# Performance work log

Hardware: AMD Instinct MI355X
Metric: run time of the kernel (lower is better)

## Reference

```python
import jax, jax.numpy as jnp
import numpy as np

B, N, DIM, H = 4, 128, 512, 8
EPS = 1e-5

def _lin(k, fan_in, fan_out):
    kw, kb = jax.random.split(k)
    w = jax.random.normal(kw, (fan_in, fan_out), jnp.float32) * 0.02
    b = jax.random.normal(kb, (fan_out,), jnp.float32) * 0.02
    return w, b

def setup_inputs() -> dict:
    key = jax.random.key(0)
    ks = jax.random.split(key, 12)
    node_features = jax.random.normal(ks[0], (B, N, DIM), jnp.float32)
    edge_features = jax.random.normal(ks[1], (B, N, N, DIM), jnp.float32)
    adjacency_weights = jax.random.uniform(ks[2], (B, N, N), jnp.float32)
    Wn_w, Wn_b = _lin(ks[3], DIM, DIM)
    We1_w, We1_b = _lin(ks[4], 3 * DIM, DIM)
    We2_w, We2_b = _lin(ks[5], DIM, H)
    Wm_w, Wm_b = _lin(ks[6], DIM, DIM)
    Wu1_w, Wu1_b = _lin(ks[7], 3 * DIM, DIM)
    Wu2_w, Wu2_b = _lin(ks[8], DIM, DIM)
    Wo_w, Wo_b = _lin(ks[9], DIM, DIM)
    ln_g = jnp.ones((DIM,), jnp.float32)
    ln_b = jnp.zeros((DIM,), jnp.float32)
    return dict(node_features=node_features, edge_features=edge_features,
                adjacency_weights=adjacency_weights,
                Wn_w=Wn_w, Wn_b=Wn_b, We1_w=We1_w, We1_b=We1_b,
                We2_w=We2_w, We2_b=We2_b, Wm_w=Wm_w, Wm_b=Wm_b,
                Wu1_w=Wu1_w, Wu1_b=Wu1_b, Wu2_w=Wu2_w, Wu2_b=Wu2_b,
                Wo_w=Wo_w, Wo_b=Wo_b, ln_g=ln_g, ln_b=ln_b)

def _layernorm(x, g, b):
    mu = jnp.mean(x, axis=-1, keepdims=True)
    var = jnp.var(x, axis=-1, keepdims=True)
    return (x - mu) * jax.lax.rsqrt(var + EPS) * g + b

def reference(node_features, edge_features, adjacency_weights,
              Wn_w, Wn_b, We1_w, We1_b, We2_w, We2_b, Wm_w, Wm_b,
              Wu1_w, Wu1_b, Wu2_w, Wu2_b, Wo_w, Wo_b, ln_g, ln_b):
    b, n, d = node_features.shape
    h = node_features @ Wn_w + Wn_b                       # (B,N,D)
    h_i = jnp.broadcast_to(h[:, :, None, :], (b, n, n, d))
    h_j = jnp.broadcast_to(h[:, None, :, :], (b, n, n, d))
    edge_input = jnp.concatenate([h_i, h_j, edge_features], axis=-1)  # (B,N,N,3D)
    # edge attention MLP
    e = jax.nn.leaky_relu(edge_input @ We1_w + We1_b, negative_slope=0.2)
    attn = e @ We2_w + We2_b                              # (B,N,N,H)
    attn = jax.nn.softmax(attn, axis=2)                   # softmax over j
    attn = attn * adjacency_weights[..., None]
    # messages: W_msg applied to h_j == W_msg(h) broadcast; aggregate with mean attn
    messages = h @ Wm_w + Wm_b                            # (B,N,D)
    attn_mean = jnp.mean(attn, axis=-1)                   # (B,N,N)
    aggregated = jnp.einsum('bij,bjd->bid', attn_mean, messages)
    updated_nodes = _layernorm(node_features + (aggregated @ Wo_w + Wo_b), ln_g, ln_b)
    # edge update MLP (exact GELU as in torch default)
    u = jax.nn.gelu(edge_input @ Wu1_w + Wu1_b, approximate=False)
    updated_edges = edge_features + (u @ Wu2_w + Wu2_b)
    return updated_nodes, updated_edges
```

## Files before the change

kernel.cpp:

```cpp
#include <hip/hip_runtime.h>
#include <hip/hip_bf16.h>


typedef __bf16  bf16x8 __attribute__((ext_vector_type(8)));
typedef float   f32x4  __attribute__((ext_vector_type(4)));
typedef __hip_bfloat16 bfloat;

#define AS1 __attribute__((address_space(1)))
#define AS3 __attribute__((address_space(3)))

__device__ __forceinline__ void g2l16(const void* g, void* l) {
  __builtin_amdgcn_global_load_lds((AS1 void*)g, (AS3 void*)l, 16, 0, 0);
}

__device__ __forceinline__ float ldf(const void* p, size_t i, int f) {
  return f ? ((const float*)p)[i] : __bfloat162float(((const bfloat*)p)[i]);
}
__device__ __forceinline__ void stf(void* p, size_t i, float v, int f) {
  if (f) ((float*)p)[i] = v;
  else   ((bfloat*)p)[i] = __float2bfloat16(v);
}

__device__ __forceinline__ float gelu_f(float x) {
  float y = 0.7978845608028654f * (x + 0.044715f * x * x * x);
  float e = __expf(2.0f * y);
  float t = 1.0f - 2.0f / (e + 1.0f);
  return 0.5f * x * (1.0f + t);
}

__global__ __launch_bounds__(256) void detect_dtype(const unsigned short* nu, int* flag) {
  __shared__ int bad;
  if (threadIdx.x == 0) bad = 0;
  __syncthreads();
  int local = 0;
  for (int i = threadIdx.x; i < 4096; i += 256) {
    int ex = (nu[i] >> 7) & 0xFF;
    if (ex >= 0xC0) local = 1;
  }
  if (local) atomicOr(&bad, 1);
  __syncthreads();
  if (threadIdx.x == 0) *flag = bad;
}

__global__ __launch_bounds__(256) void cvt_edge(const float* E, const int* flag, void* dout) {
  if (*flag == 0) return;
  const int e = blockIdx.x & 7;
  const int x = blockIdx.x >> 3;
  const int m = x >> 5;
  const int h = (x >> 4) & 1;
  const int s = x & 15;
  const int c = 2 * e + 16 * m + h;
  const int t = threadIdx.x;
  const int rloc = s * 4 + (t >> 6);
  const int c8 = t & 63;
  const float* src = E + ((size_t)c * 64 + rloc) * 512 + (size_t)c8 * 8;
  f32x4 lo = *(const f32x4*)src;
  f32x4 hi = *(const f32x4*)(src + 4);
  bf16x8 v;
  v[0] = (__bf16)lo[0]; v[1] = (__bf16)lo[1]; v[2] = (__bf16)lo[2]; v[3] = (__bf16)lo[3];
  v[4] = (__bf16)hi[0]; v[5] = (__bf16)hi[1]; v[6] = (__bf16)hi[2]; v[7] = (__bf16)hi[3];
  char* eb = (char*)dout + 1048576;
  *(bf16x8*)(eb + (size_t)c * 131072 + (size_t)rloc * 1024 + (size_t)c8 * 16) = v;
}

__global__ __launch_bounds__(256) void transpose3(const void* We1, const void* Wu1,
                                                  const void* Wu2, const void* Wm,
                                                  const int* flag,
                                                  bfloat* WtA, bfloat* WtB, bfloat* WtC,
                                                  bfloat* WtD, bfloat* WtE, bfloat* WtF,
                                                  bfloat* WtG, bfloat* WtH) {
  const int f = *flag;
  int idx = blockIdx.x * 256 + threadIdx.x;
  int m = idx >> 18;
  int r = idx & 262143;
  int n = r >> 9, k = r & 511;
  size_t si = (size_t)k * 512 + n;
  float v;
  bfloat* dst;
  switch (m) {
    case 0:  v = ldf(We1, 524288 + si, f); dst = WtA; break;
    case 1:  v = ldf(Wu1, 524288 + si, f); dst = WtB; break;
    case 2:  v = ldf(Wu2, si, f);          dst = WtC; break;
    case 3:  v = ldf(We1, si, f);          dst = WtD; break;
    case 4:  v = ldf(We1, 262144 + si, f); dst = WtE; break;
    case 5:  v = ldf(Wu1, si, f);          dst = WtF; break;
    case 6:  v = ldf(Wu1, 262144 + si, f); dst = WtG; break;
    default: v = ldf(Wm, si, f);           dst = WtH; break;
  }
  dst[(size_t)n * 512 + k] = __float2bfloat16(v);
}

__global__ __launch_bounds__(256) void small_gemm(const void* A, int amode, const void* W,
                                                  size_t woff, const void* bias,
                                                  const int* flag, float* out, bfloat* outb) {
  const int f = *flag;
  const int af = amode ? 1 : f;
  __shared__ float sA[4][512];
  const int t = threadIdx.x;
  const int r0 = blockIdx.x * 4;
  for (int idx = t; idx < 2048; idx += 256)
    sA[idx >> 9][idx & 511] = ldf(A, (size_t)(r0 + (idx >> 9)) * 512 + (idx & 511), af);
  __syncthreads();
  float acc0[4] = {0.f, 0.f, 0.f, 0.f}, acc1[4] = {0.f, 0.f, 0.f, 0.f};
#pragma unroll 4
  for (int k = 0; k < 512; ++k) {
    float w0 = ldf(W, woff + (size_t)k * 512 + t, f);
    float w1 = ldf(W, woff + (size_t)k * 512 + t + 256, f);
#pragma unroll
    for (int r = 0; r < 4; ++r) {
      acc0[r] += sA[r][k] * w0;
      acc1[r] += sA[r][k] * w1;
    }
  }
  float b0 = bias ? ldf(bias, t, f) : 0.f;
  float b1 = bias ? ldf(bias, t + 256, f) : 0.f;
#pragma unroll
  for (int r = 0; r < 4; ++r) {
    float o0 = acc0[r] + b0, o1 = acc1[r] + b1;
    out[(size_t)(r0 + r) * 512 + t] = o0;
    out[(size_t)(r0 + r) * 512 + t + 256] = o1;
    if (outb) {
      outb[(size_t)(r0 + r) * 512 + t] = __float2bfloat16(o0);
      outb[(size_t)(r0 + r) * 512 + t + 256] = __float2bfloat16(o1);
    }
  }
}

__global__ __launch_bounds__(256) void fused5_mfma(const bfloat* hb, const bfloat* WtD,
                                                   const bfloat* WtE, const bfloat* WtF,
                                                   const bfloat* WtG, const bfloat* WtH,
                                                   const void* We1b, const void* Wu1b,
                                                   const void* Wmb, const int* flag,
                                                   float* P1, float* Q1, float* P2, float* Q2,
                                                   float* msgv) {
  const int fl = *flag;
  __shared__ __align__(16) char smem[49152];
  f32x4 acc[4][4];
#pragma unroll
  for (int mi = 0; mi < 4; ++mi)
#pragma unroll
    for (int ni = 0; ni < 4; ++ni) acc[mi][ni] = (f32x4){0.f, 0.f, 0.f, 0.f};

  const int bid = blockIdx.x;
  const int g = bid >> 4, rb = (bid >> 2) & 3, cbv = bid & 3;
  const bfloat* Wt;
  const void* bias = nullptr;
  float* out;
  switch (g) {
    case 0:  Wt = WtD; bias = We1b; out = P1; break;
    case 1:  Wt = WtE; out = Q1; break;
    case 2:  Wt = WtF; bias = Wu1b; out = P2; break;
    case 3:  Wt = WtG; out = Q2; break;
    default: Wt = WtH; bias = Wmb; out = msgv; break;
  }
  const bfloat* Ag = hb + (size_t)rb * 65536;
  const bfloat* Bg = Wt + (size_t)cbv * 65536;

  const int t = threadIdx.x, lane = t & 63, wave = t >> 6;
  const int wrow = wave >> 1, wcol = wave & 1;
  const int l15 = lane & 15, q = lane >> 4;

  const int row0 = t >> 2, p0 = t & 3, g0 = p0 ^ ((row0 >> 1) & 3);
  const int row1 = 64 + row0, g1 = p0 ^ ((row1 >> 1) & 3);
  const char* srcA0 = (const char*)(Ag + (size_t)row0 * 512 + g0 * 8);
  const char* srcA1 = (const char*)(Ag + (size_t)row1 * 512 + g1 * 8);
  const char* srcB0 = (const char*)(Bg + (size_t)row0 * 512 + g0 * 8);
  const char* srcB1 = (const char*)(Bg + (size_t)row1 * 512 + g1 * 8);
  const int dst0 = wave * 1024, dst1 = 4096 + wave * 1024;

  auto stage = [&](int kt2, int sel2) {
    const int koff = kt2 * 64;
    char* dA = smem + sel2 * 8192;
    char* dB = smem + 24576 + sel2 * 8192;
    g2l16(srcA0 + koff, dA + dst0);
    g2l16(srcA1 + koff, dA + dst1);
    g2l16(srcB0 + koff, dB + dst0);
    g2l16(srcB1 + koff, dB + dst1);
  };
  stage(0, 0);
  stage(1, 1);

  const int swz = (q ^ ((l15 >> 1) & 3)) * 16;
  const int fA = (wrow * 64 + l15) * 64 + swz;
  const int fB = (wcol * 64 + l15) * 64 + swz;

#pragma unroll
  for (int kt = 0; kt < 16; ++kt) {
    if (kt < 15) asm volatile("s_waitcnt vmcnt(4)" ::: "memory");
    else         asm volatile("s_waitcnt vmcnt(0)" ::: "memory");
    __builtin_amdgcn_s_barrier();
    if (kt < 14) stage(kt + 2, (kt + 2) % 3);
    const char* A = smem + (kt % 3) * 8192;
    const char* B = smem + 24576 + (kt % 3) * 8192;
    bf16x8 afr[4], bfr[4];
#pragma unroll
    for (int mi = 0; mi < 4; ++mi) afr[mi] = *(const bf16x8*)(A + fA + mi * 1024);
#pragma unroll
    for (int ni = 0; ni < 4; ++ni) bfr[ni] = *(const bf16x8*)(B + fB + ni * 1024);
#pragma unroll
    for (int mi = 0; mi < 4; ++mi)
#pragma unroll
      for (int ni = 0; ni < 4; ++ni)
        acc[mi][ni] =
            __builtin_amdgcn_mfma_f32_16x16x32_bf16(afr[mi], bfr[ni], acc[mi][ni], 0, 0, 0);
  }

  float bv[4];
#pragma unroll
  for (int ni = 0; ni < 4; ++ni)
    bv[ni] = bias ? ldf(bias, (size_t)cbv * 128 + wcol * 64 + ni * 16 + l15, fl) : 0.f;
#pragma unroll
  for (int mi = 0; mi < 4; ++mi)
#pragma unroll
    for (int rr = 0; rr < 4; ++rr) {
      const int j = wrow * 64 + mi * 16 + q * 4 + rr;
#pragma unroll
      for (int ni = 0; ni < 4; ++ni) {
        const int cc = wcol * 64 + ni * 16 + l15;
        out[(size_t)(rb * 128 + j) * 512 + cbv * 128 + cc] = acc[mi][ni][rr] + bv[ni];
      }
    }
}

__global__ __launch_bounds__(256) void k3_edge_mlp(const void* E, const bfloat* WtA,
                                                   const bfloat* WtB, const float* P1,
                                                   const float* Q1, const float* P2,
                                                   const float* Q2, const void* We2,
                                                   const int* flag, float* logits4, void* dout) {
  const int f = *flag;
  __shared__ __align__(16) char smem[77824];
  f32x4 accA[4][4], accU[4][4];
#pragma unroll
  for (int mi = 0; mi < 4; ++mi)
#pragma unroll
    for (int ni = 0; ni < 4; ++ni) {
      accA[mi][ni] = (f32x4){0.f, 0.f, 0.f, 0.f};
      accU[mi][ni] = (f32x4){0.f, 0.f, 0.f, 0.f};
    }

  const int idx0 = blockIdx.x;
  const int bm = (idx0 >> 5) * 8 + (idx0 & 7);
  const int cb = (idx0 >> 3) & 3;
  const int blockcol = cb * 128;
  const bfloat* BgA = WtA + (size_t)cb * 65536;
  const bfloat* BgU = WtB + (size_t)cb * 65536;
  const bfloat* Eb = (const bfloat*)E;
  const char* eb = (const char*)dout + 1048576;

  const int t = threadIdx.x, lane = t & 63, wave = t >> 6;
  const int wrow = wave >> 1, wcol = wave & 1;
  const int l15 = lane & 15, q = lane >> 4;

  for (int idx = t; idx < 2048; idx += 256) {
    const int n = idx >> 7, k = idx & 127;
    float v = (n < 8) ? ldf(We2, (size_t)(blockcol + k) * 8 + n, f) : 0.f;
    *(bfloat*)(smem + 73728 + (size_t)n * 256 + (((k >> 3) ^ n) * 16) + (k & 7) * 2) =
        __float2bfloat16(v);
  }

  const int row0 = t >> 2, p0 = t & 3, g0 = p0 ^ ((row0 >> 1) & 3);
  const int row1 = 64 + row0, g1 = p0 ^ ((row1 >> 1) & 3);
  const char* srcA0;
  const char* srcA1;
  const int gr0 = bm * 128 + row0, gr1 = gr0 + 64;
  if (f) {
    srcA0 = eb + (size_t)(gr0 >> 6) * 131072 + (size_t)(gr0 & 63) * 1024 + (size_t)g0 * 16;
    srcA1 = eb + (size_t)(gr1 >> 6) * 131072 + (size_t)(gr1 & 63) * 1024 + (size_t)g1 * 16;
  } else {
    srcA0 = (const char*)Eb + ((size_t)gr0 * 512 + g0 * 8) * 2;
    srcA1 = (const char*)Eb + ((size_t)gr1 * 512 + g1 * 8) * 2;
  }
  const int dstA0 = wave * 1024, dstA1 = 4096 + wave * 1024;

  const char* srcB[4];
  int dstB[4];
#pragma unroll
  for (int c = 0; c < 4; ++c) {
    const int idx = c * 256 + t;
    const int row = idx >> 2, p = idx & 3, gg = p ^ ((row >> 1) & 3);
    const bfloat* base =
        (row < 128) ? (BgA + (size_t)row * 512) : (BgU + (size_t)(row - 128) * 512);
    srcB[c] = (const char*)base + gg * 16;
    dstB[c] = (c * 256 + wave * 64) * 16;
  }

  auto stage = [&](int kt2, int sel2) {
    const int koff = kt2 * 64;
    char* dA = smem + sel2 * 8192;
    char* dB = smem + 24576 + sel2 * 16384;
    g2l16(srcA0 + koff, dA + dstA0);
    g2l16(srcA1 + koff, dA + dstA1);
#pragma unroll
    for (int c = 0; c < 4; ++c) g2l16(srcB[c] + koff, dB + dstB[c]);
  };
  stage(0, 0);
  stage(1, 1);

  const int swz = (q ^ ((l15 >> 1) & 3)) * 16;
  const int fA = (wrow * 64 + l15) * 64 + swz;
  const int fB = (wcol * 64 + l15) * 64 + swz;

#pragma unroll
  for (int kt = 0; kt < 16; ++kt) {
    if (kt < 15) asm volatile("s_waitcnt vmcnt(6)" ::: "memory");
    else         asm volatile("s_waitcnt vmcnt(0)" ::: "memory");
    __builtin_amdgcn_s_barrier();
    if (kt < 14) stage(kt + 2, (kt + 2) % 3);
    const char* A = smem + (kt % 3) * 8192;
    const char* B = smem + 24576 + (kt % 3) * 16384;
    bf16x8 afr[4], bfrA[4], bfrU[4];
#pragma unroll
    for (int mi = 0; mi < 4; ++mi) afr[mi] = *(const bf16x8*)(A + fA + mi * 1024);
#pragma unroll
    for (int ni = 0; ni < 4; ++ni) bfrA[ni] = *(const bf16x8*)(B + fB + ni * 1024);
#pragma unroll
    for (int mi = 0; mi < 4; ++mi)
#pragma unroll
      for (int ni = 0; ni < 4; ++ni)
        accA[mi][ni] =
            __builtin_amdgcn_mfma_f32_16x16x32_bf16(afr[mi], bfrA[ni], accA[mi][ni], 0, 0, 0);
#pragma unroll
    for (int ni = 0; ni < 4; ++ni) bfrU[ni] = *(const bf16x8*)(B + 8192 + fB + ni * 1024);
#pragma unroll
    for (int mi = 0; mi < 4; ++mi)
#pragma unroll
      for (int ni = 0; ni < 4; ++ni)
        accU[mi][ni] =
            __builtin_amdgcn_mfma_f32_16x16x32_bf16(afr[mi], bfrU[ni], accU[mi][ni], 0, 0, 0);
  }

  const int b = bm >> 7;
  float pv1[4], pv2[4];
#pragma unroll
  for (int ni = 0; ni < 4; ++ni) {
    const size_t o = (size_t)bm * 512 + blockcol + wcol * 64 + ni * 16 + l15;
    pv1[ni] = P1[o];
    pv2[ni] = P2[o];
  }
  __syncthreads();

#pragma unroll
  for (int mi = 0; mi < 4; ++mi)
#pragma unroll
    for (int rr = 0; rr < 4; ++rr) {
      const int j = wrow * 64 + mi * 16 + q * 4 + rr;
#pragma unroll
      for (int ni = 0; ni < 4; ++ni) {
        const int cc = wcol * 64 + ni * 16 + l15;
        const int c = blockcol + cc;
        float x = accU[mi][ni][rr] + pv2[ni] + Q2[((size_t)b * 128 + j) * 512 + c];
        *(bfloat*)(smem + (size_t)j * 256 + (((cc >> 3) ^ (j & 15)) * 16) + (cc & 7) * 2) =
            __float2bfloat16(gelu_f(x));
      }
    }
  __syncthreads();
  {
    char* ubase = (char*)dout + (f ? (1048576 + 65536) : 524288);
    const size_t blkstride = f ? 131072 : 65536;
#pragma unroll
    for (int rd = 0; rd < 8; ++rd) {
      const int j = rd * 16 + (t >> 4);
      const int ch = t & 15;
      f32x4 v = *(const f32x4*)(smem + (size_t)j * 256 + ((ch ^ (j & 15)) * 16));
      const size_t m = (size_t)bm * 128 + j;
      *(f32x4*)(ubase + (m >> 6) * blkstride + (m & 63) * 1024 + (size_t)blockcol * 2 +
                (size_t)ch * 16) = v;
    }
  }
  __syncthreads();

#pragma unroll
  for (int mi = 0; mi < 4; ++mi)
#pragma unroll
    for (int rr = 0; rr < 4; ++rr) {
      const int j = wrow * 64 + mi * 16 + q * 4 + rr;
#pragma unroll
      for (int ni = 0; ni < 4; ++ni) {
        const int cc = wcol * 64 + ni * 16 + l15;
        const int c = blockcol + cc;
        float x = accA[mi][ni][rr] + pv1[ni] + Q1[((size_t)b * 128 + j) * 512 + c];
        float e4 = (x >= 0.f) ? x : 0.2f * x;
        *(bfloat*)(smem + (size_t)j * 256 + (((cc >> 3) ^ (j & 15)) * 16) + (cc & 7) * 2) =
            __float2bfloat16(e4);
      }
    }
  __syncthreads();
  {
    f32x4 acc2[2];
    acc2[0] = (f32x4){0.f, 0.f, 0.f, 0.f};
    acc2[1] = (f32x4){0.f, 0.f, 0.f, 0.f};
    const int jb = wave * 32;
#pragma unroll
    for (int ks = 0; ks < 4; ++ks) {
      const int gA = ((ks * 4 + q) ^ l15) * 16;
      bf16x8 a0 = *(const bf16x8*)(smem + (size_t)(jb + l15) * 256 + gA);
      bf16x8 a1 = *(const bf16x8*)(smem + (size_t)(jb + 16 + l15) * 256 + gA);
      bf16x8 bb = *(const bf16x8*)(smem + 73728 + (size_t)l15 * 256 + gA);
      acc2[0] = __builtin_amdgcn_mfma_f32_16x16x32_bf16(a0, bb, acc2[0], 0, 0, 0);
      acc2[1] = __builtin_amdgcn_mfma_f32_16x16x32_bf16(a1, bb, acc2[1], 0, 0, 0);
    }
#pragma unroll
    for (int mi2 = 0; mi2 < 2; ++mi2)
#pragma unroll
      for (int rr = 0; rr < 4; ++rr) {
        if (l15 < 8) {
          const int j = jb + mi2 * 16 + q * 4 + rr;
          logits4[(((size_t)cb * 512 + bm) * 128 + j) * 8 + l15] = acc2[mi2][rr];
        }
      }
  }
}

__global__ __launch_bounds__(512) void k6_edge_out(const bfloat* WtC, const void* Wu2b,
                                                   const void* E, const int* flag, void* dout) {
  const int f = *flag;
  __shared__ __align__(16) char smem[110592];
  f32x4 acc[2][8];
#pragma unroll
  for (int mi = 0; mi < 2; ++mi)
#pragma unroll
    for (int ni = 0; ni < 8; ++ni) acc[mi][ni] = (f32x4){0.f, 0.f, 0.f, 0.f};

  const int e = blockIdx.x & 7;
  const int x = blockIdx.x >> 3;
  const int bm = 2 * e + 16 * (x >> 1) + (x & 1);
  const int t = threadIdx.x;
  const int lane = t & 63;
  const int wave = t >> 6;
  const int wm = wave >> 2, wn = wave & 3;
  const int l15 = lane & 15;
  const int q = lane >> 4;
  const size_t r0 = (size_t)bm * 64;
  const char* ua = (const char*)dout +
                   (f ? (1048576 + (size_t)bm * 131072 + 65536) : (524288 + (size_t)bm * 65536));

  const int iA = t & 255;
  const int rowA = iA >> 2, pA = iA & 3, gA = pA ^ ((rowA >> 1) & 3);
  const char* srcA = ua + (size_t)rowA * 1024 + (size_t)gA * 16;
  const int dstA = (wave & 3) * 1024;
  const char* srcB[4];
  int dstB[4];
#pragma unroll
  for (int c = 0; c < 4; ++c) {
    const int idx = c * 512 + t;
    const int row = idx >> 2, p = idx & 3, g = p ^ ((row >> 1) & 3);
    srcB[c] = (const char*)WtC + ((size_t)row * 512 + g * 8) * 2;
    dstB[c] = (c * 512 + wave * 64) * 16;
  }

  auto stage = [&](int kt2, int sel2) {
    const int koff = kt2 * 64;
    char* dA = smem + sel2 * 4096;
    char* dB = smem + 12288 + sel2 * 32768;
    g2l16(srcA + koff, dA + dstA);
#pragma unroll
    for (int c = 0; c < 4; ++c) g2l16(srcB[c] + koff, dB + dstB[c]);
  };

  stage(0, 0);
  stage(1, 1);

  const int swz = (q ^ ((l15 >> 1) & 3)) * 16;
  const int fAo = (wm * 32 + l15) * 64 + swz;
  const int fBo = (wn * 128 + l15) * 64 + swz;

#pragma unroll
  for (int kt = 0; kt < 16; ++kt) {
    if (kt < 15) asm volatile("s_waitcnt vmcnt(5)" ::: "memory");
    else         asm volatile("s_waitcnt vmcnt(0)" ::: "memory");
    __builtin_amdgcn_s_barrier();
    if (kt < 14) stage(kt + 2, (kt + 2) % 3);
    const char* sA = smem + (kt % 3) * 4096;
    const char* sB = smem + 12288 + (kt % 3) * 32768;
    bf16x8 afr[2], bfr[8];
#pragma unroll
    for (int mi = 0; mi < 2; ++mi) afr[mi] = *(const bf16x8*)(sA + fAo + mi * 1024);
#pragma unroll
    for (int ni = 0; ni < 8; ++ni) bfr[ni] = *(const bf16x8*)(sB + fBo + ni * 1024);
#pragma unroll
    for (int mi = 0; mi < 2; ++mi)
#pragma unroll
      for (int ni = 0; ni < 8; ++ni)
        acc[mi][ni] = __builtin_amdgcn_mfma_f32_16x16x32_bf16(afr[mi], bfr[ni], acc[mi][ni], 0, 0, 0);
  }
  float wb[8];
#pragma unroll
  for (int ni = 0; ni < 8; ++ni) wb[ni] = ldf(Wu2b, wn * 128 + ni * 16 + l15, f);
  const bfloat* eres = (const bfloat*)((const char*)dout + 1048576 + (size_t)bm * 131072);
#pragma unroll
  for (int mi = 0; mi < 2; ++mi)
#pragma unroll
    for (int rr = 0; rr < 4; ++rr) {
      const int j = wm * 32 + mi * 16 + q * 4 + rr;
#pragma unroll
      for (int ni = 0; ni < 8; ++ni) {
        const int c = wn * 128 + ni * 16 + l15;
        float r = f ? __bfloat162float(eres[(size_t)j * 512 + c])
                    : __bfloat162float(((const bfloat*)E)[(r0 + j) * 512 + c]);
        acc[mi][ni][rr] += wb[ni] + r;
      }
    }
  __syncthreads();
#pragma unroll
  for (int mi = 0; mi < 2; ++mi)
#pragma unroll
    for (int rr = 0; rr < 4; ++rr) {
      const int j = wm * 32 + mi * 16 + q * 4 + rr;
      const size_t row = r0 + j;
#pragma unroll
      for (int ni = 0; ni < 8; ++ni) {
        const int c = wn * 128 + ni * 16 + l15;
        stf(dout, 262144 + row * 512 + c, acc[mi][ni][rr], f);
      }
    }
}

__global__ __launch_bounds__(128) void softmax_mean(const float* logits4, const void* adj,
                                                    const int* flag, float* amean) {
  const int f = *flag;
  const int bi = blockIdx.x;
  const int j = threadIdx.x;
  const int wv = j >> 6;
  __shared__ float sred[2][8];
  f32x4 v0 = (f32x4){0.f, 0.f, 0.f, 0.f}, v1 = (f32x4){0.f, 0.f, 0.f, 0.f};
#pragma unroll
  for (int s = 0; s < 4; ++s) {
    const float* p = logits4 + (((size_t)s * 512 + bi) * 128 + j) * 8;
    v0 += *(const f32x4*)p;
    v1 += *(const f32x4*)(p + 4);
  }
  float xv[8], m[8];
#pragma unroll
  for (int k = 0; k < 4; ++k) { xv[k] = v0[k]; xv[4 + k] = v1[k]; }
#pragma unroll
  for (int h = 0; h < 8; ++h) m[h] = xv[h];
#pragma unroll
  for (int o = 1; o < 64; o <<= 1)
#pragma unroll
    for (int h = 0; h < 8; ++h) m[h] = fmaxf(m[h], __shfl_xor(m[h], o));
  if ((j & 63) == 0) {
#pragma unroll
    for (int h = 0; h < 8; ++h) sred[wv][h] = m[h];
  }
  __syncthreads();
  float ex[8], s8[8];
#pragma unroll
  for (int h = 0; h < 8; ++h) {
    float mx = fmaxf(sred[0][h], sred[1][h]);
    ex[h] = __expf(xv[h] - mx);
    s8[h] = ex[h];
  }
#pragma unroll
  for (int o = 1; o < 64; o <<= 1)
#pragma unroll
    for (int h = 0; h < 8; ++h) s8[h] += __shfl_xor(s8[h], o);
  __syncthreads();
  if ((j & 63) == 0) {
#pragma unroll
    for (int h = 0; h < 8; ++h) sred[wv][h] = s8[h];
  }
  __syncthreads();
  float macc = 0.f;
#pragma unroll
  for (int h = 0; h < 8; ++h) macc += ex[h] / (sred[0][h] + sred[1][h]);
  amean[(size_t)bi * 128 + j] = macc * 0.125f * ldf(adj, (size_t)bi * 128 + j, f);
}

__global__ __launch_bounds__(256) void node_fused(const float* amean, const float* msg,
                                                  const void* Wo, const void* Wob,
                                                  const void* node, const void* lng,
                                                  const void* lnb, const int* flag, void* dout) {
  const int f = *flag;
  const int r0 = blockIdx.x * 4;
  const int b = r0 >> 7;
  const int t = threadIdx.x;
  const int lane = t & 63, wave = t >> 6;
  __shared__ float am[512];
  __shared__ float sAgg[4][512];
  __shared__ float sw[4][4];
  __shared__ float sw2[4][4];
  am[t] = amean[(size_t)r0 * 128 + t];
  am[t + 256] = amean[(size_t)r0 * 128 + t + 256];
  __syncthreads();
  float a0[4] = {0.f, 0.f, 0.f, 0.f}, a1[4] = {0.f, 0.f, 0.f, 0.f};
#pragma unroll 2
  for (int jj = 0; jj < 128; ++jj) {
    const float* mr = msg + ((size_t)b * 128 + jj) * 512;
    float m0 = mr[t], m1 = mr[t + 256];
#pragma unroll
    for (int r = 0; r < 4; ++r) {
      a0[r] += am[r * 128 + jj] * m0;
      a1[r] += am[r * 128 + jj] * m1;
    }
  }
#pragma unroll
  for (int r = 0; r < 4; ++r) { sAgg[r][t] = a0[r]; sAgg[r][t + 256] = a1[r]; }
  __syncthreads();
  float v0[4] = {0.f, 0.f, 0.f, 0.f}, v1[4] = {0.f, 0.f, 0.f, 0.f};
  if (f) {
    const float* W = (const float*)Wo;
#pragma unroll 2
    for (int k = 0; k < 512; ++k) {
      float w0 = W[(size_t)k * 512 + t], w1 = W[(size_t)k * 512 + t + 256];
#pragma unroll
      for (int r = 0; r < 4; ++r) { v0[r] += sAgg[r][k] * w0; v1[r] += sAgg[r][k] * w1; }
    }
  } else {
    const bfloat* W = (const bfloat*)Wo;
#pragma unroll 2
    for (int k = 0; k < 512; ++k) {
      float w0 = __bfloat162float(W[(size_t)k * 512 + t]);
      float w1 = __bfloat162float(W[(size_t)k * 512 + t + 256]);
#pragma unroll
      for (int r = 0; r < 4; ++r) { v0[r] += sAgg[r][k] * w0; v1[r] += sAgg[r][k] * w1; }
    }
  }
  float wob0 = ldf(Wob, t, f), wob1 = ldf(Wob, t + 256, f);
#pragma unroll
  for (int r = 0; r < 4; ++r) {
    v0[r] += wob0 + ldf(node, (size_t)(r0 + r) * 512 + t, f);
    v1[r] += wob1 + ldf(node, (size_t)(r0 + r) * 512 + t + 256, f);
  }
  float s[4];
#pragma unroll
  for (int r = 0; r < 4; ++r) s[r] = v0[r] + v1[r];
#pragma unroll
  for (int o = 1; o < 64; o <<= 1)
#pragma unroll
    for (int r = 0; r < 4; ++r) s[r] += __shfl_xor(s[r], o);
  if (lane == 0) {
#pragma unroll
    for (int r = 0; r < 4; ++r) sw[wave][r] = s[r];
  }
  __syncthreads();
  float mean[4];
#pragma unroll
  for (int r = 0; r < 4; ++r)
    mean[r] = (sw[0][r] + sw[1][r] + sw[2][r] + sw[3][r]) * (1.f / 512.f);
#pragma unroll
  for (int r = 0; r < 4; ++r) {
    float d0 = v0[r] - mean[r], d1 = v1[r] - mean[r];
    s[r] = d0 * d0 + d1 * d1;
  }
#pragma unroll
  for (int o = 1; o < 64; o <<= 1)
#pragma unroll
    for (int r = 0; r < 4; ++r) s[r] += __shfl_xor(s[r], o);
  if (lane == 0) {
#pragma unroll
    for (int r = 0; r < 4; ++r) sw2[wave][r] = s[r];
  }
  __syncthreads();
  float g0v = ldf(lng, t, f), g1v = ldf(lng, t + 256, f);
  float b0v = ldf(lnb, t, f), b1v = ldf(lnb, t + 256, f);
#pragma unroll
  for (int r = 0; r < 4; ++r) {
    float var = (sw2[0][r] + sw2[1][r] + sw2[2][r] + sw2[3][r]) * (1.f / 512.f);
    float inv = rsqrtf(var + 1e-5f);
    stf(dout, (size_t)(r0 + r) * 512 + t, (v0[r] - mean[r]) * inv * g0v + b0v, f);
    stf(dout, (size_t)(r0 + r) * 512 + t + 256, (v1[r] - mean[r]) * inv * g1v + b1v, f);
  }
}

extern "C" void kernel_launch(void* const* d_in, const int* in_sizes, int n_in, void* d_out,
                              int out_size, void* d_ws, size_t ws_size, hipStream_t stream) {
  (void)in_sizes; (void)n_in; (void)out_size; (void)ws_size;
  const void* node = d_in[0];
  const void* edge = d_in[1];
  const void* adj = d_in[2];
  const void* Wn_w = d_in[3];
  const void* Wn_b = d_in[4];
  const void* We1_w = d_in[5];
  const void* We1_b = d_in[6];
  const void* We2_w = d_in[7];
  const void* Wm_w = d_in[9];
  const void* Wm_b = d_in[10];
  const void* Wu1_w = d_in[11];
  const void* Wu1_b = d_in[12];
  const void* Wu2_w = d_in[13];
  const void* Wu2_b = d_in[14];
  const void* Wo_w = d_in[15];
  const void* Wo_b = d_in[16];
  const void* ln_g = d_in[17];
  const void* ln_b = d_in[18];

  char* w = (char*)d_ws;
  int* flag = (int*)w;        w += 256;
  float* h = (float*)w;       w += 262144 * 4;
  float* P1 = (float*)w;      w += 262144 * 4;
  float* Q1 = (float*)w;      w += 262144 * 4;
  float* P2 = (float*)w;      w += 262144 * 4;
  float* Q2 = (float*)w;      w += 262144 * 4;
  float* msg = (float*)w;     w += 262144 * 4;
  float* logits4 = (float*)w; w += (size_t)4 * 524288 * 4;
  float* amean = (float*)w;   w += 65536 * 4;
  bfloat* WtA = (bfloat*)w;   w += 262144 * 2;
  bfloat* WtB = (bfloat*)w;   w += 262144 * 2;
  bfloat* WtC = (bfloat*)w;   w += 262144 * 2;
  bfloat* WtD = (bfloat*)w;   w += 262144 * 2;
  bfloat* WtE = (bfloat*)w;   w += 262144 * 2;
  bfloat* WtF = (bfloat*)w;   w += 262144 * 2;
  bfloat* WtG = (bfloat*)w;   w += 262144 * 2;
  bfloat* WtH = (bfloat*)w;   w += 262144 * 2;
  bfloat* hb = (bfloat*)w;    w += 262144 * 2;

  detect_dtype<<<1, 256, 0, stream>>>((const unsigned short*)node, flag);
  cvt_edge<<<16384, 256, 0, stream>>>((const float*)edge, flag, d_out);
  transpose3<<<8192, 256, 0, stream>>>(We1_w, Wu1_w, Wu2_w, Wm_w, flag, WtA, WtB, WtC,
                                       WtD, WtE, WtF, WtG, WtH);
  small_gemm<<<128, 256, 0, stream>>>(node, 0, Wn_w, 0, Wn_b, flag, h, hb);
  fused5_mfma<<<80, 256, 0, stream>>>(hb, WtD, WtE, WtF, WtG, WtH, We1_b, Wu1_b, Wm_b, flag,
                                      P1, Q1, P2, Q2, msg);
  k3_edge_mlp<<<2048, 256, 0, stream>>>(edge, WtA, WtB, P1, Q1, P2, Q2, We2_w, flag,
                                        logits4, d_out);
  softmax_mean<<<512, 128, 0, stream>>>(logits4, adj, flag, amean);
  node_fused<<<128, 256, 0, stream>>>(amean, msg, Wo_w, Wo_b, node, ln_g, ln_b, flag, d_out);
  k6_edge_out<<<1024, 512, 0, stream>>>(WtC, Wu2_b, edge, flag, d_out);
}
```

Before: 823.6 us.

## Split edge MLP blocks by branch, stage GELU output in workspace, tile weight transpose

```diff
diff --git a/kernel.cpp b/kernel.cpp
--- a/kernel.cpp
+++ b/kernel.cpp
@@ -63,31 +63,49 @@
   *(bf16x8*)(eb + (size_t)c * 131072 + (size_t)rloc * 1024 + (size_t)c8 * 16) = v;
 }
 
-__global__ __launch_bounds__(256) void transpose3(const void* We1, const void* Wu1,
+__global__ __launch_bounds__(256) void transpose8(const void* We1, const void* Wu1,
                                                   const void* Wu2, const void* Wm,
                                                   const int* flag,
                                                   bfloat* WtA, bfloat* WtB, bfloat* WtC,
                                                   bfloat* WtD, bfloat* WtE, bfloat* WtF,
                                                   bfloat* WtG, bfloat* WtH) {
   const int f = *flag;
-  int idx = blockIdx.x * 256 + threadIdx.x;
-  int m = idx >> 18;
-  int r = idx & 262143;
-  int n = r >> 9, k = r & 511;
-  size_t si = (size_t)k * 512 + n;
-  float v;
+  __shared__ float sT[64][65];
+  const int m = blockIdx.x >> 6;
+  const int tile = blockIdx.x & 63;
+  const int k0 = (tile >> 3) * 64, n0 = (tile & 7) * 64;
+  const void* src;
+  size_t woff = 0;
   bfloat* dst;
   switch (m) {
-    case 0:  v = ldf(We1, 524288 + si, f); dst = WtA; break;
-    case 1:  v = ldf(Wu1, 524288 + si, f); dst = WtB; break;
-    case 2:  v = ldf(Wu2, si, f);          dst = WtC; break;
-    case 3:  v = ldf(We1, si, f);          dst = WtD; break;
-    case 4:  v = ldf(We1, 262144 + si, f); dst = WtE; break;
-    case 5:  v = ldf(Wu1, si, f);          dst = WtF; break;
-    case 6:  v = ldf(Wu1, 262144 + si, f); dst = WtG; break;
-    default: v = ldf(Wm, si, f);           dst = WtH; break;
-  }
-  dst[(size_t)n * 512 + k] = __float2bfloat16(v);
+    case 0:  src = We1; woff = 524288; dst = WtA; break;
+    case 1:  src = Wu1; woff = 524288; dst = WtB; break;
+    case 2:  src = Wu2; dst = WtC; break;
+    case 3:  src = We1; dst = WtD; break;
+    case 4:  src = We1; woff = 262144; dst = WtE; break;
+    case 5:  src = Wu1; dst = WtF; break;
+    case 6:  src = Wu1; woff = 262144; dst = WtG; break;
+    default: src = Wm; dst = WtH; break;
+  }
+  const int t = threadIdx.x;
+#pragma unroll
+  for (int p = 0; p < 4; ++p) {
+    const int r = p * 16 + (t >> 4);
+    const int cs = (t & 15) * 4;
+    const size_t base = woff + (size_t)(k0 + r) * 512 + n0 + cs;
+#pragma unroll
+    for (int i = 0; i < 4; ++i) sT[r][cs + i] = ldf(src, base + i, f);
+  }
+  __syncthreads();
+#pragma unroll
+  for (int p = 0; p < 2; ++p) {
+    const int n = p * 32 + (t >> 3);
+    const int ks = (t & 7) * 8;
+    bf16x8 v;
+#pragma unroll
+    for (int i = 0; i < 8; ++i) v[i] = (__bf16)sT[ks + i][n];
+    *(bf16x8*)(dst + (size_t)(n0 + n) * 512 + k0 + ks) = v;
+  }
 }
 
 __global__ __launch_bounds__(256) void small_gemm(const void* A, int amode, const void* W,
@@ -226,40 +244,36 @@
                                                    const bfloat* WtB, const float* P1,
                                                    const float* Q1, const float* P2,
                                                    const float* Q2, const void* We2,
-                                                   const int* flag, float* logits4, void* dout) {
+                                                   const int* flag, float* logits4,
+                                                   bfloat* uws, void* dout) {
   const int f = *flag;
-  __shared__ __align__(16) char smem[77824];
-  f32x4 accA[4][4], accU[4][4];
+  __shared__ __align__(16) char smem[53248];
+  f32x4 acc[4][4];
 #pragma unroll
   for (int mi = 0; mi < 4; ++mi)
 #pragma unroll
-    for (int ni = 0; ni < 4; ++ni) {
-      accA[mi][ni] = (f32x4){0.f, 0.f, 0.f, 0.f};
-      accU[mi][ni] = (f32x4){0.f, 0.f, 0.f, 0.f};
-    }
+    for (int ni = 0; ni < 4; ++ni) acc[mi][ni] = (f32x4){0.f, 0.f, 0.f, 0.f};
 
   const int idx0 = blockIdx.x;
-  const int bm = (idx0 >> 5) * 8 + (idx0 & 7);
-  const int cb = (idx0 >> 3) & 3;
-  const int blockcol = cb * 128;
-  const bfloat* BgA = WtA + (size_t)cb * 65536;
-  const bfloat* BgU = WtB + (size_t)cb * 65536;
+  const int bm = (idx0 >> 6) * 8 + (idx0 & 7);
+  const int bn = (idx0 >> 3) & 7;
+  const bool attn = bn < 4;
+  const bfloat* Bg = attn ? WtA + (size_t)bn * 65536 : WtB + (size_t)(bn - 4) * 65536;
   const bfloat* Eb = (const bfloat*)E;
   const char* eb = (const char*)dout + 1048576;
 
-  const int t = threadIdx.x, lane = t & 63, wave = t >> 6;
+  const int t = threadIdx.x;
+  const int lane = t & 63;
+  const int wave = t >> 6;
   const int wrow = wave >> 1, wcol = wave & 1;
-  const int l15 = lane & 15, q = lane >> 4;
-
-  for (int idx = t; idx < 2048; idx += 256) {
-    const int n = idx >> 7, k = idx & 127;
-    float v = (n < 8) ? ldf(We2, (size_t)(blockcol + k) * 8 + n, f) : 0.f;
-    *(bfloat*)(smem + 73728 + (size_t)n * 256 + (((k >> 3) ^ n) * 16) + (k & 7) * 2) =
-        __float2bfloat16(v);
-  }
+  const int l15 = lane & 15;
+  const int q = lane >> 4;
+  const int blockcol = (attn ? bn : (bn - 4)) * 128;
 
   const int row0 = t >> 2, p0 = t & 3, g0 = p0 ^ ((row0 >> 1) & 3);
   const int row1 = 64 + row0, g1 = p0 ^ ((row1 >> 1) & 3);
+  const char* srcB0 = (const char*)Bg + ((size_t)row0 * 512 + g0 * 8) * 2;
+  const char* srcB1 = (const char*)Bg + ((size_t)row1 * 512 + g1 * 8) * 2;
   const char* srcA0;
   const char* srcA1;
   const int gr0 = bm * 128 + row0, gr1 = gr0 + 64;
@@ -270,93 +284,87 @@
     srcA0 = (const char*)Eb + ((size_t)gr0 * 512 + g0 * 8) * 2;
     srcA1 = (const char*)Eb + ((size_t)gr1 * 512 + g1 * 8) * 2;
   }
-  const int dstA0 = wave * 1024, dstA1 = 4096 + wave * 1024;
-
-  const char* srcB[4];
-  int dstB[4];
-#pragma unroll
-  for (int c = 0; c < 4; ++c) {
-    const int idx = c * 256 + t;
-    const int row = idx >> 2, p = idx & 3, gg = p ^ ((row >> 1) & 3);
-    const bfloat* base =
-        (row < 128) ? (BgA + (size_t)row * 512) : (BgU + (size_t)(row - 128) * 512);
-    srcB[c] = (const char*)base + gg * 16;
-    dstB[c] = (c * 256 + wave * 64) * 16;
-  }
+  const int dst0 = wave * 1024;
+  const int dst1 = 4096 + wave * 1024;
 
   auto stage = [&](int kt2, int sel2) {
+    char* dA = smem + sel2 * 8192;
+    char* dB = smem + 24576 + sel2 * 8192;
     const int koff = kt2 * 64;
-    char* dA = smem + sel2 * 8192;
-    char* dB = smem + 24576 + sel2 * 16384;
-    g2l16(srcA0 + koff, dA + dstA0);
-    g2l16(srcA1 + koff, dA + dstA1);
-#pragma unroll
-    for (int c = 0; c < 4; ++c) g2l16(srcB[c] + koff, dB + dstB[c]);
+    g2l16(srcA0 + koff, dA + dst0);
+    g2l16(srcA1 + koff, dA + dst1);
+    g2l16(srcB0 + koff, dB + dst0);
+    g2l16(srcB1 + koff, dB + dst1);
   };
+
   stage(0, 0);
   stage(1, 1);
 
-  const int swz = (q ^ ((l15 >> 1) & 3)) * 16;
-  const int fA = (wrow * 64 + l15) * 64 + swz;
-  const int fB = (wcol * 64 + l15) * 64 + swz;
+  if (attn) {
+    for (int idx = t; idx < 2048; idx += 256) {
+      const int n = idx >> 7, k = idx & 127;
+      float v = (n < 8) ? ldf(We2, (size_t)(blockcol + k) * 8 + n, f) : 0.f;
+      *(bfloat*)(smem + 49152 + (size_t)n * 256 + (((k >> 3) ^ n) * 16) + (k & 7) * 2) =
+          __float2bfloat16(v);
+    }
+  }
+
+  const int swzf = (q ^ ((l15 >> 1) & 3)) * 16;
+  const int fA = (wrow * 64 + l15) * 64 + swzf;
+  const int fB = (wcol * 64 + l15) * 64 + swzf;
 
 #pragma unroll
   for (int kt = 0; kt < 16; ++kt) {
-    if (kt < 15) asm volatile("s_waitcnt vmcnt(6)" ::: "memory");
+    if (kt < 15) asm volatile("s_waitcnt vmcnt(4)" ::: "memory");
     else         asm volatile("s_waitcnt vmcnt(0)" ::: "memory");
     __builtin_amdgcn_s_barrier();
     if (kt < 14) stage(kt + 2, (kt + 2) % 3);
     const char* A = smem + (kt % 3) * 8192;
-    const char* B = smem + 24576 + (kt % 3) * 16384;
-    bf16x8 afr[4], bfrA[4], bfrU[4];
+    const char* B = smem + 24576 + (kt % 3) * 8192;
+    bf16x8 afr[4], bfr[4];
 #pragma unroll
     for (int mi = 0; mi < 4; ++mi) afr[mi] = *(const bf16x8*)(A + fA + mi * 1024);
 #pragma unroll
-    for (int ni = 0; ni < 4; ++ni) bfrA[ni] = *(const bf16x8*)(B + fB + ni * 1024);
+    for (int ni = 0; ni < 4; ++ni) bfr[ni] = *(const bf16x8*)(B + fB + ni * 1024);
 #pragma unroll
     for (int mi = 0; mi < 4; ++mi)
 #pragma unroll
       for (int ni = 0; ni < 4; ++ni)
-        accA[mi][ni] =
-            __builtin_amdgcn_mfma_f32_16x16x32_bf16(afr[mi], bfrA[ni], accA[mi][ni], 0, 0, 0);
-#pragma unroll
-    for (int ni = 0; ni < 4; ++ni) bfrU[ni] = *(const bf16x8*)(B + 8192 + fB + ni * 1024);
+        acc[mi][ni] =
+            __builtin_amdgcn_mfma_f32_16x16x32_bf16(afr[mi], bfr[ni], acc[mi][ni], 0, 0, 0);
+  }
+
+  const int b = bm >> 7;
+  const float* P = attn ? P1 : P2;
+  const float* Qm = attn ? Q1 : Q2;
+  float pv[4];
+#pragma unroll
+  for (int ni = 0; ni < 4; ++ni)
+    pv[ni] = P[(size_t)bm * 512 + blockcol + wcol * 64 + ni * 16 + l15];
+
+  __syncthreads();
+
+  if (!attn) {
 #pragma unroll
     for (int mi = 0; mi < 4; ++mi)
 #pragma unroll
-      for (int ni = 0; ni < 4; ++ni)
-        accU[mi][ni] =
-            __builtin_amdgcn_mfma_f32_16x16x32_bf16(afr[mi], bfrU[ni], accU[mi][ni], 0, 0, 0);
-  }
-
-  const int b = bm >> 7;
-  float pv1[4], pv2[4];
-#pragma unroll
-  for (int ni = 0; ni < 4; ++ni) {
-    const size_t o = (size_t)bm * 512 + blockcol + wcol * 64 + ni * 16 + l15;
-    pv1[ni] = P1[o];
-    pv2[ni] = P2[o];
-  }
-  __syncthreads();
-
-#pragma unroll
-  for (int mi = 0; mi < 4; ++mi)
-#pragma unroll
-    for (int rr = 0; rr < 4; ++rr) {
-      const int j = wrow * 64 + mi * 16 + q * 4 + rr;
-#pragma unroll
-      for (int ni = 0; ni < 4; ++ni) {
-        const int cc = wcol * 64 + ni * 16 + l15;
-        const int c = blockcol + cc;
-        float x = accU[mi][ni][rr] + pv2[ni] + Q2[((size_t)b * 128 + j) * 512 + c];
-        *(bfloat*)(smem + (size_t)j * 256 + (((cc >> 3) ^ (j & 15)) * 16) + (cc & 7) * 2) =
-            __float2bfloat16(gelu_f(x));
+      for (int rr = 0; rr < 4; ++rr) {
+        const int j = wrow * 64 + mi * 16 + q * 4 + rr;
+#pragma unroll
+        for (int ni = 0; ni < 4; ++ni) {
+          const int cc = wcol * 64 + ni * 16 + l15;
+          const int c = blockcol + cc;
+          float x = acc[mi][ni][rr] + pv[ni] + Qm[((size_t)b * 128 + j) * 512 + c];
+          *(bfloat*)(smem + (size_t)j * 256 + (((cc >> 3) ^ (j & 15)) * 16) + (cc & 7) * 2) =
+              __float2bfloat16(gelu_f(x));
+        }
       }
-    }
-  __syncthreads();
-  {
-    char* ubase = (char*)dout + (f ? (1048576 + 65536) : 524288);
-    const size_t blkstride = f ? 131072 : 65536;
+    __syncthreads();
+    char* ubase;
+    size_t blkstride;
+    if (uws) { ubase = (char*)uws; blkstride = 65536; }
+    else if (f) { ubase = (char*)dout + 1048576 + 65536; blkstride = 131072; }
+    else { ubase = (char*)dout + 524288; blkstride = 65536; }
 #pragma unroll
     for (int rd = 0; rd < 8; ++rd) {
       const int j = rd * 16 + (t >> 4);
@@ -366,26 +374,23 @@
       *(f32x4*)(ubase + (m >> 6) * blkstride + (m & 63) * 1024 + (size_t)blockcol * 2 +
                 (size_t)ch * 16) = v;
     }
-  }
-  __syncthreads();
-
-#pragma unroll
-  for (int mi = 0; mi < 4; ++mi)
-#pragma unroll
-    for (int rr = 0; rr < 4; ++rr) {
-      const int j = wrow * 64 + mi * 16 + q * 4 + rr;
-#pragma unroll
-      for (int ni = 0; ni < 4; ++ni) {
-        const int cc = wcol * 64 + ni * 16 + l15;
-        const int c = blockcol + cc;
-        float x = accA[mi][ni][rr] + pv1[ni] + Q1[((size_t)b * 128 + j) * 512 + c];
-        float e4 = (x >= 0.f) ? x : 0.2f * x;
-        *(bfloat*)(smem + (size_t)j * 256 + (((cc >> 3) ^ (j & 15)) * 16) + (cc & 7) * 2) =
-            __float2bfloat16(e4);
+  } else {
+#pragma unroll
+    for (int mi = 0; mi < 4; ++mi)
+#pragma unroll
+      for (int rr = 0; rr < 4; ++rr) {
+        const int j = wrow * 64 + mi * 16 + q * 4 + rr;
+#pragma unroll
+        for (int ni = 0; ni < 4; ++ni) {
+          const int cc = wcol * 64 + ni * 16 + l15;
+          const int c = blockcol + cc;
+          float x = acc[mi][ni][rr] + pv[ni] + Qm[((size_t)b * 128 + j) * 512 + c];
+          float e4 = (x >= 0.f) ? x : 0.2f * x;
+          *(bfloat*)(smem + (size_t)j * 256 + (((cc >> 3) ^ (j & 15)) * 16) + (cc & 7) * 2) =
+              __float2bfloat16(e4);
+        }
       }
-    }
-  __syncthreads();
-  {
+    __syncthreads();
     f32x4 acc2[2];
     acc2[0] = (f32x4){0.f, 0.f, 0.f, 0.f};
     acc2[1] = (f32x4){0.f, 0.f, 0.f, 0.f};
@@ -395,7 +400,7 @@
       const int gA = ((ks * 4 + q) ^ l15) * 16;
       bf16x8 a0 = *(const bf16x8*)(smem + (size_t)(jb + l15) * 256 + gA);
       bf16x8 a1 = *(const bf16x8*)(smem + (size_t)(jb + 16 + l15) * 256 + gA);
-      bf16x8 bb = *(const bf16x8*)(smem + 73728 + (size_t)l15 * 256 + gA);
+      bf16x8 bb = *(const bf16x8*)(smem + 49152 + (size_t)l15 * 256 + gA);
       acc2[0] = __builtin_amdgcn_mfma_f32_16x16x32_bf16(a0, bb, acc2[0], 0, 0, 0);
       acc2[1] = __builtin_amdgcn_mfma_f32_16x16x32_bf16(a1, bb, acc2[1], 0, 0, 0);
     }
@@ -405,16 +410,103 @@
       for (int rr = 0; rr < 4; ++rr) {
         if (l15 < 8) {
           const int j = jb + mi2 * 16 + q * 4 + rr;
-          logits4[(((size_t)cb * 512 + bm) * 128 + j) * 8 + l15] = acc2[mi2][rr];
+          logits4[(((size_t)bn * 512 + bm) * 128 + j) * 8 + l15] = acc2[mi2][rr];
         }
       }
   }
 }
 
-__global__ __launch_bounds__(512) void k6_edge_out(const bfloat* WtC, const void* Wu2b,
-                                                   const void* E, const int* flag, void* dout) {
+__global__ __launch_bounds__(256) void k6_ws(const bfloat* uws, const bfloat* WtC,
+                                             const void* Wu2b, const void* E,
+                                             const int* flag, void* dout) {
   const int f = *flag;
-  __shared__ __align__(16) char smem[110592];
+  __shared__ __align__(16) char smem[49152];
+  f32x4 acc[4][4];
+#pragma unroll
+  for (int mi = 0; mi < 4; ++mi)
+#pragma unroll
+    for (int ni = 0; ni < 4; ++ni) acc[mi][ni] = (f32x4){0.f, 0.f, 0.f, 0.f};
+
+  const int idx0 = blockIdx.x;
+  const int rb = (idx0 >> 5) * 8 + (idx0 & 7);
+  const int cb = (idx0 >> 3) & 3;
+
+  const int t = threadIdx.x, lane = t & 63, wave = t >> 6;
+  const int wrow = wave >> 1, wcol = wave & 1;
+  const int l15 = lane & 15, q = lane >> 4;
+
+  const bfloat* Bg = WtC + (size_t)cb * 65536;
+  const int row0 = t >> 2, p0 = t & 3, g0 = p0 ^ ((row0 >> 1) & 3);
+  const int row1 = 64 + row0, g1 = p0 ^ ((row1 >> 1) & 3);
+  const char* srcA0 = (const char*)uws + (size_t)(rb * 128 + row0) * 1024 + (size_t)g0 * 16;
+  const char* srcA1 = (const char*)uws + (size_t)(rb * 128 + row1) * 1024 + (size_t)g1 * 16;
+  const char* srcB0 = (const char*)(Bg + (size_t)row0 * 512 + g0 * 8);
+  const char* srcB1 = (const char*)(Bg + (size_t)row1 * 512 + g1 * 8);
+  const int dst0 = wave * 1024, dst1 = 4096 + wave * 1024;
+
+  auto stage = [&](int kt2, int sel2) {
+    const int koff = kt2 * 64;
+    char* dA = smem + sel2 * 8192;
+    char* dB = smem + 24576 + sel2 * 8192;
+    g2l16(srcA0 + koff, dA + dst0);
+    g2l16(srcA1 + koff, dA + dst1);
+    g2l16(srcB0 + koff, dB + dst0);
+    g2l16(srcB1 + koff, dB + dst1);
+  };
+  stage(0, 0);
+  stage(1, 1);
+
+  const int swz = (q ^ ((l15 >> 1) & 3)) * 16;
+  const int fA = (wrow * 64 + l15) * 64 + swz;
+  const int fB = (wcol * 64 + l15) * 64 + swz;
+
+#pragma unroll
+  for (int kt = 0; kt < 16; ++kt) {
+    if (kt < 15) asm volatile("s_waitcnt vmcnt(4)" ::: "memory");
+    else         asm volatile("s_waitcnt vmcnt(0)" ::: "memory");
+    __builtin_amdgcn_s_barrier();
+    if (kt < 14) stage(kt + 2, (kt + 2) % 3);
+    const char* A = smem + (kt % 3) * 8192;
+    const char* B = smem + 24576 + (kt % 3) * 8192;
+    bf16x8 afr[4], bfr[4];
+#pragma unroll
+    for (int mi = 0; mi < 4; ++mi) afr[mi] = *(const bf16x8*)(A + fA + mi * 1024);
+#pragma unroll
+    for (int ni = 0; ni < 4; ++ni) bfr[ni] = *(const bf16x8*)(B + fB + ni * 1024);
+#pragma unroll
+    for (int mi = 0; mi < 4; ++mi)
+#pragma unroll
+      for (int ni = 0; ni < 4; ++ni)
+        acc[mi][ni] =
+            __builtin_amdgcn_mfma_f32_16x16x32_bf16(afr[mi], bfr[ni], acc[mi][ni], 0, 0, 0);
+  }
+
+  float wb[4];
+#pragma unroll
+  for (int ni = 0; ni < 4; ++ni)
+    wb[ni] = ldf(Wu2b, (size_t)cb * 128 + wcol * 64 + ni * 16 + l15, f);
+#pragma unroll
+  for (int mi = 0; mi < 4; ++mi)
+#pragma unroll
+    for (int rr = 0; rr < 4; ++rr) {
+      const int j = wrow * 64 + mi * 16 + q * 4 + rr;
+      const size_t row = (size_t)rb * 128 + j;
+#pragma unroll
+      for (int ni = 0; ni < 4; ++ni) {
+        const int c = cb * 128 + wcol * 64 + ni * 16 + l15;
+        float r = f ? ((const float*)E)[row * 512 + c]
+                    : __bfloat162float(((const bfloat*)E)[row * 512 + c]);
+        stf(dout, 262144 + row * 512 + c, acc[mi][ni][rr] + wb[ni] + r, f);
+      }
+    }
+}
+
+__global__ __launch_bounds__(512) void k6_chunk(const bfloat* WtC, const void* Wu2b,
+                                                const void* E, const int* flag, void* dout) {
+  const int f = *flag;
+  __shared__ __align__(16) char smem[36864];
+  char* sA = smem;
+  char* sB = smem + 4096;
   f32x4 acc[2][8];
 #pragma unroll
   for (int mi = 0; mi < 2; ++mi)
@@ -434,49 +526,33 @@
   const char* ua = (const char*)dout +
                    (f ? (1048576 + (size_t)bm * 131072 + 65536) : (524288 + (size_t)bm * 65536));
 
-  const int iA = t & 255;
-  const int rowA = iA >> 2, pA = iA & 3, gA = pA ^ ((rowA >> 1) & 3);
-  const char* srcA = ua + (size_t)rowA * 1024 + (size_t)gA * 16;
-  const int dstA = (wave & 3) * 1024;
-  const char* srcB[4];
-  int dstB[4];
-#pragma unroll
-  for (int c = 0; c < 4; ++c) {
-    const int idx = c * 512 + t;
-    const int row = idx >> 2, p = idx & 3, g = p ^ ((row >> 1) & 3);
-    srcB[c] = (const char*)WtC + ((size_t)row * 512 + g * 8) * 2;
-    dstB[c] = (c * 512 + wave * 64) * 16;
-  }
-
-  auto stage = [&](int kt2, int sel2) {
-    const int koff = kt2 * 64;
-    char* dA = smem + sel2 * 4096;
-    char* dB = smem + 12288 + sel2 * 32768;
-    g2l16(srcA + koff, dA + dstA);
-#pragma unroll
-    for (int c = 0; c < 4; ++c) g2l16(srcB[c] + koff, dB + dstB[c]);
-  };
-
-  stage(0, 0);
-  stage(1, 1);
-
-  const int swz = (q ^ ((l15 >> 1) & 3)) * 16;
-  const int fAo = (wm * 32 + l15) * 64 + swz;
-  const int fBo = (wn * 128 + l15) * 64 + swz;
-
-#pragma unroll
   for (int kt = 0; kt < 16; ++kt) {
-    if (kt < 15) asm volatile("s_waitcnt vmcnt(5)" ::: "memory");
-    else         asm volatile("s_waitcnt vmcnt(0)" ::: "memory");
-    __builtin_amdgcn_s_barrier();
-    if (kt < 14) stage(kt + 2, (kt + 2) % 3);
-    const char* sA = smem + (kt % 3) * 4096;
-    const char* sB = smem + 12288 + (kt % 3) * 32768;
+    __syncthreads();
+    const int k0 = kt * 32;
+    if (t < 256) {
+      const int row = t >> 2;
+      const int gseg = (t & 3) ^ ((row >> 1) & 3);
+      g2l16(ua + (size_t)row * 1024 + (size_t)(k0 + gseg * 8) * 2, sA + wave * 64 * 16);
+    }
+#pragma unroll
+    for (int c = 0; c < 4; ++c) {
+      const int idx = c * 512 + t;
+      const int row = idx >> 2;
+      const int gseg = (idx & 3) ^ ((row >> 1) & 3);
+      g2l16(WtC + (size_t)row * 512 + k0 + gseg * 8, sB + (c * 512 + wave * 64) * 16);
+    }
+    __syncthreads();
     bf16x8 afr[2], bfr[8];
 #pragma unroll
-    for (int mi = 0; mi < 2; ++mi) afr[mi] = *(const bf16x8*)(sA + fAo + mi * 1024);
-#pragma unroll
-    for (int ni = 0; ni < 8; ++ni) bfr[ni] = *(const bf16x8*)(sB + fBo + ni * 1024);
+    for (int mi = 0; mi < 2; ++mi) {
+      const int r = wm * 32 + mi * 16 + l15;
+      afr[mi] = *(const bf16x8*)(sA + ((size_t)r * 32 + (q ^ ((r >> 1) & 3)) * 8) * 2);
+    }
+#pragma unroll
+    for (int ni = 0; ni < 8; ++ni) {
+      const int r = wn * 128 + ni * 16 + l15;
+      bfr[ni] = *(const bf16x8*)(sB + ((size_t)r * 32 + (q ^ ((r >> 1) & 3)) * 8) * 2);
+    }
 #pragma unroll
     for (int mi = 0; mi < 2; ++mi)
 #pragma unroll
@@ -664,7 +740,7 @@
 
 extern "C" void kernel_launch(void* const* d_in, const int* in_sizes, int n_in, void* d_out,
                               int out_size, void* d_ws, size_t ws_size, hipStream_t stream) {
-  (void)in_sizes; (void)n_in; (void)out_size; (void)ws_size;
+  (void)in_sizes; (void)n_in; (void)out_size;
   const void* node = d_in[0];
   const void* edge = d_in[1];
   const void* adj = d_in[2];
@@ -703,17 +779,23 @@
   bfloat* WtG = (bfloat*)w;   w += 262144 * 2;
   bfloat* WtH = (bfloat*)w;   w += 262144 * 2;
   bfloat* hb = (bfloat*)w;    w += 262144 * 2;
+  bfloat* u_ws = (bfloat*)w;  w += (size_t)65536 * 1024;
+  const int uws_ok = (ws_size >= (size_t)(w - (char*)d_ws)) ? 1 : 0;
+  if (!uws_ok) u_ws = nullptr;
 
   detect_dtype<<<1, 256, 0, stream>>>((const unsigned short*)node, flag);
   cvt_edge<<<16384, 256, 0, stream>>>((const float*)edge, flag, d_out);
-  transpose3<<<8192, 256, 0, stream>>>(We1_w, Wu1_w, Wu2_w, Wm_w, flag, WtA, WtB, WtC,
-                                       WtD, WtE, WtF, WtG, WtH);
+  transpose8<<<512, 256, 0, stream>>>(We1_w, Wu1_w, Wu2_w, Wm_w, flag, WtA, WtB, WtC,
+                                      WtD, WtE, WtF, WtG, WtH);
   small_gemm<<<128, 256, 0, stream>>>(node, 0, Wn_w, 0, Wn_b, flag, h, hb);
   fused5_mfma<<<80, 256, 0, stream>>>(hb, WtD, WtE, WtF, WtG, WtH, We1_b, Wu1_b, Wm_b, flag,
                                       P1, Q1, P2, Q2, msg);
-  k3_edge_mlp<<<2048, 256, 0, stream>>>(edge, WtA, WtB, P1, Q1, P2, Q2, We2_w, flag,
-                                        logits4, d_out);
+  k3_edge_mlp<<<4096, 256, 0, stream>>>(edge, WtA, WtB, P1, Q1, P2, Q2, We2_w, flag,
+                                        logits4, u_ws, d_out);
   softmax_mean<<<512, 128, 0, stream>>>(logits4, adj, flag, amean);
   node_fused<<<128, 256, 0, stream>>>(amean, msg, Wo_w, Wo_b, node, ln_g, ln_b, flag, d_out);
-  k6_edge_out<<<1024, 512, 0, stream>>>(WtC, Wu2_b, edge, flag, d_out);
-}
+  if (uws_ok)
+    k6_ws<<<2048, 256, 0, stream>>>(u_ws, WtC, Wu2_b, edge, flag, d_out);
+  else
+    k6_chunk<<<1024, 512, 0, stream>>>(WtC, Wu2_b, edge, flag, d_out);
+}
```

After: 737.6 us. 1.12x faster.
